# Optimization experiments

Hardware: AMD Instinct MI355X
Metric: run time of the kernel (lower is better)

The kernel has to match this reference:

```python
import jax, jax.numpy as jnp
import numpy as np

N_HEADS = 8
EMBED = 640
CROSS = 768
HEAD = EMBED // N_HEADS


def setup_inputs() -> dict:
    key = jax.random.key(0)
    ks = jax.random.split(key, 10)
    s_e = 1.0 / np.sqrt(EMBED)
    s_c = 1.0 / np.sqrt(CROSS)
    return {
        "x": jax.random.normal(ks[0], (8, 4096, EMBED), jnp.float32),
        "y": jax.random.normal(ks[1], (8, 77, CROSS), jnp.float32),
        "Wq": jax.random.uniform(ks[2], (EMBED, EMBED), jnp.float32, -s_e, s_e),
        "bq": jax.random.uniform(ks[3], (EMBED,), jnp.float32, -s_e, s_e),
        "Wk": jax.random.uniform(ks[4], (CROSS, EMBED), jnp.float32, -s_c, s_c),
        "bk": jax.random.uniform(ks[5], (EMBED,), jnp.float32, -s_c, s_c),
        "Wv": jax.random.uniform(ks[6], (CROSS, EMBED), jnp.float32, -s_c, s_c),
        "bv": jax.random.uniform(ks[7], (EMBED,), jnp.float32, -s_c, s_c),
        "Wo": jax.random.uniform(ks[8], (EMBED, EMBED), jnp.float32, -s_e, s_e),
        "bo": jax.random.uniform(ks[9], (EMBED,), jnp.float32, -s_e, s_e),
    }


def reference(x, y, Wq, bq, Wk, bk, Wv, bv, Wo, bo):
    B, T, C = x.shape
    S = y.shape[1]
    # projections; split heads: [B, H, T, D]
    q = (x @ Wq + bq).reshape(B, T, N_HEADS, HEAD).transpose(0, 2, 1, 3)
    k = (y @ Wk + bk).reshape(B, S, N_HEADS, HEAD).transpose(0, 2, 1, 3)
    v = (y @ Wv + bv).reshape(B, S, N_HEADS, HEAD).transpose(0, 2, 1, 3)
    scores = jnp.einsum("bhtd,bhsd->bhts", q, k) / jnp.sqrt(jnp.float32(HEAD))
    attn = jax.nn.softmax(scores, axis=-1)
    out = jnp.einsum("bhts,bhsd->bhtd", attn, v)
    out = out.transpose(0, 2, 1, 3).reshape(B, T, C)
    return out @ Wo + bo
```

## Files before the change

kernel.cpp:

```cpp
#include <hip/hip_runtime.h>
#include <hip/hip_bf16.h>
#include <hip/hip_fp16.h>

#define EMBED 640
#define CROSS 768
#define NH 8
#define HEAD 80
#define BATCH 8
#define SEQT 4096
#define SEQS 77
#define MROWS (BATCH * SEQT)

typedef _Float16 half8 __attribute__((ext_vector_type(8)));
typedef float floatx4 __attribute__((ext_vector_type(4)));

__device__ __forceinline__ void lds_load16(const void* g, void* l) {
    __builtin_amdgcn_global_load_lds(
        (const __attribute__((address_space(1))) void*)g,
        (__attribute__((address_space(3))) void*)l, 16, 0, 0);
}

__global__ __launch_bounds__(256) void cvt_f32_f16(
    const float* __restrict__ in, _Float16* __restrict__ out)
{
    size_t i = ((size_t)blockIdx.x * 256 + threadIdx.x) * 8;
    float4 a = *(const float4*)&in[i];
    float4 b = *(const float4*)&in[i + 4];
    half8 h;
    h[0] = (_Float16)a.x; h[1] = (_Float16)a.y;
    h[2] = (_Float16)a.z; h[3] = (_Float16)a.w;
    h[4] = (_Float16)b.x; h[5] = (_Float16)b.y;
    h[6] = (_Float16)b.z; h[7] = (_Float16)b.w;
    *(half8*)&out[i] = h;
}

__global__ __launch_bounds__(256) void cvt_y_f16(
    const float* __restrict__ y, _Float16* __restrict__ yh)
{
    size_t i = ((size_t)blockIdx.x * 256 + threadIdx.x) * 8;
    half8 h = {};
    if (i < (size_t)BATCH * SEQS * CROSS) {
        float4 a = *(const float4*)&y[i];
        float4 b = *(const float4*)&y[i + 4];
        h[0] = (_Float16)a.x; h[1] = (_Float16)a.y;
        h[2] = (_Float16)a.z; h[3] = (_Float16)a.w;
        h[4] = (_Float16)b.x; h[5] = (_Float16)b.y;
        h[6] = (_Float16)b.z; h[7] = (_Float16)b.w;
    }
    *(half8*)&yh[i] = h;
}

__global__ __launch_bounds__(256) void zero_f16(_Float16* __restrict__ p, size_t n8)
{
    size_t i = (size_t)blockIdx.x * 256 + threadIdx.x;
    if (i < n8) *(half8*)&p[i * 8] = (half8){};
}

__global__ __launch_bounds__(256) void transpose_cvt(
    const float* __restrict__ W, _Float16* __restrict__ Wt, int K, int N)
{
    __shared__ float t[32][33];
    const int k0 = blockIdx.y * 32, n0 = blockIdx.x * 32;
    for (int r = threadIdx.y; r < 32; r += 8)
        t[r][threadIdx.x] = W[(size_t)(k0 + r) * N + n0 + threadIdx.x];
    __syncthreads();
    for (int r = threadIdx.y; r < 32; r += 8)
        Wt[(size_t)(n0 + r) * K + k0 + threadIdx.x] = (_Float16)t[threadIdx.x][r];
}

template <bool HALF_OUT>
__global__ __launch_bounds__(256) void gemm_f16(
    const _Float16* __restrict__ A,
    const _Float16* __restrict__ Bt,
    const float* __restrict__ bias,
    void* __restrict__ Cout, int M, int N, int K, float scale)
{
    __shared__ _Float16 As[3][128 * 32];
    __shared__ _Float16 Bs[3][128 * 32];

    const int tid  = threadIdx.x;
    const int wave = tid >> 6;
    const int lane = tid & 63;
    const int quad = lane >> 4;
    const int l16  = lane & 15;

    const int l   = blockIdx.y * gridDim.x + blockIdx.x;
    const int inner = l >> 3;
    const int p   = (l & 7) + 8 * (inner / gridDim.x);
    const int nt  = inner % gridDim.x;
    const int m0 = p * 128, n0 = nt * 128;
    const int wm = (wave >> 1) * 64, wn = (wave & 1) * 64;

    const int row = tid >> 2;
    const int kch = ((tid & 3) ^ ((row >> 1) & 3)) * 8;
    const int cq  = (quad ^ ((l16 >> 1) & 3)) * 8;

    const _Float16* pa0 = &A [(size_t)(m0 + row)      * K + kch];
    const _Float16* pa1 = &A [(size_t)(m0 + 64 + row) * K + kch];
    const _Float16* pb0 = &Bt[(size_t)(n0 + row)      * K + kch];
    const _Float16* pb1 = &Bt[(size_t)(n0 + 64 + row) * K + kch];

    const int NT = K / 32;

    auto stage = [&](int t) {
        const int bf = t % 3;
        const int off = t * 32;
        lds_load16(pa0 + off, &As[bf][wave * 512]);
        lds_load16(pa1 + off, &As[bf][2048 + wave * 512]);
        lds_load16(pb0 + off, &Bs[bf][wave * 512]);
        lds_load16(pb1 + off, &Bs[bf][2048 + wave * 512]);
    };
    stage(0); stage(1); stage(2);

    floatx4 acc[4][4] = {};

    for (int t = 0; t < NT; ++t) {
        const int rem = NT - 1 - t;
        if (rem >= 2)      asm volatile("s_waitcnt vmcnt(8)" ::: "memory");
        else if (rem == 1) asm volatile("s_waitcnt vmcnt(4)" ::: "memory");
        else               asm volatile("s_waitcnt vmcnt(0)" ::: "memory");
        __builtin_amdgcn_s_barrier();

        const _Float16* as = As[t % 3];
        const _Float16* bs = Bs[t % 3];
        half8 a[4], b[4];
        #pragma unroll
        for (int i = 0; i < 4; ++i)
            a[i] = *(const half8*)&as[(wm + i * 16 + l16) * 32 + cq];
        #pragma unroll
        for (int j = 0; j < 4; ++j)
            b[j] = *(const half8*)&bs[(wn + j * 16 + l16) * 32 + cq];
        #pragma unroll
        for (int i = 0; i < 4; ++i)
            #pragma unroll
            for (int j = 0; j < 4; ++j)
                acc[i][j] = __builtin_amdgcn_mfma_f32_16x16x32_f16(
                    a[i], b[j], acc[i][j], 0, 0, 0);

        asm volatile("s_waitcnt lgkmcnt(0)" ::: "memory");
        __builtin_amdgcn_s_barrier();
        if (t + 3 < NT) stage(t + 3);
    }

    float bcol[4];
    #pragma unroll
    for (int j = 0; j < 4; ++j) bcol[j] = bias[n0 + wn + j * 16 + l16];
    #pragma unroll
    for (int i = 0; i < 4; ++i)
        #pragma unroll
        for (int r = 0; r < 4; ++r) {
            const int m = m0 + wm + i * 16 + quad * 4 + r;
            #pragma unroll
            for (int j = 0; j < 4; ++j) {
                float v = (acc[i][j][r] + bcol[j]) * scale;
                const size_t off = (size_t)m * N + n0 + wn + j * 16 + l16;
                if (HALF_OUT) ((_Float16*)Cout)[off] = (_Float16)v;
                else          ((float*)Cout)[off] = v;
            }
        }
}

__global__ __launch_bounds__(256) void kv_gemm(
    const _Float16* __restrict__ yh,
    const _Float16* __restrict__ Wkt, const _Float16* __restrict__ Wvt,
    const float* __restrict__ bk, const float* __restrict__ bv,
    _Float16* __restrict__ kh, _Float16* __restrict__ vth)
{
    __shared__ _Float16 As[64 * 32];
    __shared__ _Float16 Bs[64 * 32];

    const int tid = threadIdx.x;
    const int wave = tid >> 6, lane = tid & 63;
    const int quad = lane >> 4, l16 = lane & 15;
    const int m0 = blockIdx.y * 64, n0 = blockIdx.x * 64;
    const bool isV = blockIdx.z != 0;
    const _Float16* Bt = isV ? Wvt : Wkt;
    const float* bias  = isV ? bv : bk;

    const int row = tid >> 2;
    const int kch = (tid & 3) * 8;

    floatx4 acc[4] = {};

    for (int k0 = 0; k0 < CROSS; k0 += 32) {
        lds_load16(&yh[(size_t)(m0 + row) * CROSS + k0 + kch], &As[wave * 512]);
        lds_load16(&Bt[(size_t)(n0 + row) * CROSS + k0 + kch], &Bs[wave * 512]);
        __syncthreads();
        half8 b = *(const half8*)&Bs[(wave * 16 + l16) * 32 + quad * 8];
        #pragma unroll
        for (int i = 0; i < 4; ++i) {
            half8 a = *(const half8*)&As[(i * 16 + l16) * 32 + quad * 8];
            acc[i] = __builtin_amdgcn_mfma_f32_16x16x32_f16(a, b, acc[i], 0, 0, 0);
        }
        __syncthreads();
    }

    const int n = n0 + wave * 16 + l16;
    const int h = n / HEAD, d = n % HEAD;
    const float bb = bias[n];
    #pragma unroll
    for (int i = 0; i < 4; ++i)
        #pragma unroll
        for (int r = 0; r < 4; ++r) {
            const int m = m0 + i * 16 + quad * 4 + r;
            if (m >= BATCH * SEQS) continue;
            const int b_ = m / SEQS, s = m % SEQS;
            const int bh = b_ * NH + h;
            const float v = acc[i][r] + bb;
            if (isV) vth[(size_t)bh * (HEAD * 80) + d * 80 + s] = (_Float16)v;
            else     kh [(size_t)bh * (SEQS * HEAD) + s * HEAD + d] = (_Float16)v;
        }
}

__global__ __launch_bounds__(256, 4) void attn_mfma(
    const _Float16* __restrict__ qh,
    const _Float16* __restrict__ kh,
    const _Float16* __restrict__ vth,
    _Float16* __restrict__ oh)
{
    constexpr int LS = 88;
    __shared__ _Float16 lds[(80 + 80 + 64) * LS + 8];
    _Float16* Ks = lds;
    _Float16* Vt = lds + 80 * LS;
    _Float16* Ps = lds + 160 * LS;

    const int tid = threadIdx.x;
    const int wave = tid >> 6, lane = tid & 63;
    const int quad = lane >> 4, l16 = lane & 15;
    const int bh = blockIdx.y;
    const int b = bh >> 3, h = bh & 7;
    const size_t row0 = (size_t)b * SEQT + (size_t)blockIdx.x * 256;
    const half8 hz = {};

    const _Float16* qp = qh + (row0 + wave * 16 + l16) * EMBED + h * HEAD;

    half8 qa0 = *(const half8*)&qp[quad * 8];
    half8 qa1 = *(const half8*)&qp[32 + quad * 8];
    half8 qa2 = (quad < 2) ? *(const half8*)&qp[64 + quad * 8] : hz;

    for (int idx = tid; idx < 80 * 11; idx += 256) {
        const int s = idx / 11, c = idx % 11;
        half8 v = hz;
        if (s < SEQS && c < 10)
            v = *(const half8*)&kh[(size_t)bh * (SEQS * HEAD) + s * HEAD + c * 8];
        *(half8*)&Ks[s * LS + c * 8] = v;
    }
    for (int idx = tid; idx < 80 * 11; idx += 256) {
        const int d = idx / 11, c = idx % 11;
        half8 v = hz;
        if (c < 10)
            v = *(const half8*)&vth[(size_t)bh * (HEAD * 80) + d * 80 + c * 8];
        *(half8*)&Vt[d * LS + c * 8] = v;
    }
    __syncthreads();

    for (int t = 0; t < 4; ++t) {
        floatx4 accs[5] = {};
        #pragma unroll
        for (int st = 0; st < 5; ++st) {
            const _Float16* kr = &Ks[(st * 16 + l16) * LS];
            half8 b0 = *(const half8*)&kr[quad * 8];
            half8 b1 = *(const half8*)&kr[32 + quad * 8];
            half8 b2 = *(const half8*)&kr[64 + quad * 8];
            accs[st] = __builtin_amdgcn_mfma_f32_16x16x32_f16(qa0, b0, accs[st], 0, 0, 0);
            accs[st] = __builtin_amdgcn_mfma_f32_16x16x32_f16(qa1, b1, accs[st], 0, 0, 0);
            accs[st] = __builtin_amdgcn_mfma_f32_16x16x32_f16(qa2, b2, accs[st], 0, 0, 0);
        }
        if (l16 >= 13) {
            accs[4][0] = -1e30f; accs[4][1] = -1e30f;
            accs[4][2] = -1e30f; accs[4][3] = -1e30f;
        }

        float recip[4];
        #pragma unroll
        for (int r = 0; r < 4; ++r) {
            float m = accs[0][r];
            #pragma unroll
            for (int st = 1; st < 5; ++st) m = fmaxf(m, accs[st][r]);
            m = fmaxf(m, __shfl_xor(m, 1));
            m = fmaxf(m, __shfl_xor(m, 2));
            m = fmaxf(m, __shfl_xor(m, 4));
            m = fmaxf(m, __shfl_xor(m, 8));
            float l = 0.f;
            const int row = wave * 16 + quad * 4 + r;
            #pragma unroll
            for (int st = 0; st < 5; ++st) {
                float e = __expf(accs[st][r] - m);
                l += e;
                Ps[row * LS + st * 16 + l16] = (_Float16)e;
            }
            l += __shfl_xor(l, 1);
            l += __shfl_xor(l, 2);
            l += __shfl_xor(l, 4);
            l += __shfl_xor(l, 8);
            recip[r] = 1.0f / l;
        }
        __syncthreads();

        half8 qn0 = hz, qn1 = hz, qn2 = hz;
        if (t < 3) {
            const _Float16* qn = qp + (size_t)(t + 1) * 64 * EMBED;
            qn0 = *(const half8*)&qn[quad * 8];
            qn1 = *(const half8*)&qn[32 + quad * 8];
            if (quad < 2) qn2 = *(const half8*)&qn[64 + quad * 8];
        }

        const _Float16* pr = &Ps[(wave * 16 + l16) * LS];
        half8 pa0 = *(const half8*)&pr[quad * 8];
        half8 pa1 = *(const half8*)&pr[32 + quad * 8];
        half8 pa2 = (quad < 2) ? *(const half8*)&pr[64 + quad * 8] : hz;
        __syncthreads();

        floatx4 acco[5] = {};
        #pragma unroll
        for (int dt = 0; dt < 5; ++dt) {
            const _Float16* vr = &Vt[(dt * 16 + l16) * LS];
            half8 b0 = *(const half8*)&vr[quad * 8];
            half8 b1 = *(const half8*)&vr[32 + quad * 8];
            half8 b2 = *(const half8*)&vr[64 + quad * 8];
            acco[dt] = __builtin_amdgcn_mfma_f32_16x16x32_f16(pa0, b0, acco[dt], 0, 0, 0);
            acco[dt] = __builtin_amdgcn_mfma_f32_16x16x32_f16(pa1, b1, acco[dt], 0, 0, 0);
            acco[dt] = __builtin_amdgcn_mfma_f32_16x16x32_f16(pa2, b2, acco[dt], 0, 0, 0);
        }

        #pragma unroll
        for (int r = 0; r < 4; ++r) {
            const size_t grow = row0 + t * 64 + wave * 16 + quad * 4 + r;
            #pragma unroll
            for (int dt = 0; dt < 5; ++dt)
                oh[grow * EMBED + h * HEAD + dt * 16 + l16] =
                    (_Float16)(acco[dt][r] * recip[r]);
        }

        qa0 = qn0; qa1 = qn1; qa2 = qn2;
    }
}

extern "C" void kernel_launch(void* const* d_in, const int* in_sizes, int n_in,
                              void* d_out, int out_size, void* d_ws, size_t ws_size,
                              hipStream_t stream)
{
    const float* x  = (const float*)d_in[0];
    const float* y  = (const float*)d_in[1];
    const float* Wq = (const float*)d_in[2];
    const float* bq = (const float*)d_in[3];
    const float* Wk = (const float*)d_in[4];
    const float* bk = (const float*)d_in[5];
    const float* Wv = (const float*)d_in[6];
    const float* bv = (const float*)d_in[7];
    const float* Wo = (const float*)d_in[8];
    const float* bo = (const float*)d_in[9];
    float* out = (float*)d_out;

    const size_t ME = (size_t)MROWS * EMBED;
    _Float16* xh  = (_Float16*)d_ws;
    _Float16* qh  = xh + ME;
    _Float16* ah  = qh + ME;
    _Float16* kh  = ah + ME;
    _Float16* vth = kh  + (size_t)BATCH * NH * SEQS * HEAD;
    _Float16* wqt = vth + (size_t)BATCH * NH * HEAD * 80;
    _Float16* wot = wqt + (size_t)EMBED * EMBED;
    _Float16* yh  = wot + (size_t)EMBED * EMBED;
    _Float16* wkt = yh  + (size_t)640 * CROSS;
    _Float16* wvt = wkt + (size_t)EMBED * CROSS;

    cvt_f32_f16<<<dim3(ME / (256 * 8)), 256, 0, stream>>>(x, xh);
    transpose_cvt<<<dim3(EMBED / 32, EMBED / 32), dim3(32, 8), 0, stream>>>(Wq, wqt, EMBED, EMBED);
    transpose_cvt<<<dim3(EMBED / 32, EMBED / 32), dim3(32, 8), 0, stream>>>(Wo, wot, EMBED, EMBED);
    transpose_cvt<<<dim3(EMBED / 32, CROSS / 32), dim3(32, 8), 0, stream>>>(Wk, wkt, CROSS, EMBED);
    transpose_cvt<<<dim3(EMBED / 32, CROSS / 32), dim3(32, 8), 0, stream>>>(Wv, wvt, CROSS, EMBED);
    cvt_y_f16<<<dim3(640 * CROSS / (256 * 8)), 256, 0, stream>>>(y, yh);
    zero_f16<<<dim3(((size_t)BATCH * NH * HEAD * 80 / 8 + 255) / 256), 256, 0, stream>>>(
        vth, (size_t)BATCH * NH * HEAD * 80 / 8);

    gemm_f16<true><<<dim3(EMBED / 128, MROWS / 128), 256, 0, stream>>>(
        xh, wqt, bq, qh, MROWS, EMBED, EMBED, 0.11180339887498949f);
    kv_gemm<<<dim3(EMBED / 64, 640 / 64, 2), 256, 0, stream>>>(
        yh, wkt, wvt, bk, bv, kh, vth);
    attn_mfma<<<dim3(SEQT / 256, BATCH * NH), 256, 0, stream>>>(qh, kh, vth, ah);
    gemm_f16<false><<<dim3(EMBED / 128, MROWS / 128), 256, 0, stream>>>(
        ah, wot, bo, out, MROWS, EMBED, EMBED, 1.0f);
}
```

Baseline: 301.2 us.

## Fuse x conversion into Q GEMM, merge prep kernels, reschedule GEMM pipeline

The Q projection now reads fp32 x directly, converting to fp16 in registers before writing LDS. This removes the separate conversion pass and its fp16 round trip through global memory. The four weight transposes are merged into one launch, and the y conversion is merged with the V buffer zeroing, which cuts launch count. The output GEMM now issues its next stage right after the barrier with a two-ahead prefetch and drops the second barrier per k-step. The reuse of the third buffer in that GEMM, and the register-staged A loads in gemm_q, may create hazards or stalls.

```diff
diff --git a/kernel.cpp b/kernel.cpp
--- a/kernel.cpp
+++ b/kernel.cpp
@@ -20,47 +20,22 @@
         (__attribute__((address_space(3))) void*)l, 16, 0, 0);
 }
 
-__global__ __launch_bounds__(256) void cvt_f32_f16(
-    const float* __restrict__ in, _Float16* __restrict__ out)
-{
-    size_t i = ((size_t)blockIdx.x * 256 + threadIdx.x) * 8;
-    float4 a = *(const float4*)&in[i];
-    float4 b = *(const float4*)&in[i + 4];
-    half8 h;
-    h[0] = (_Float16)a.x; h[1] = (_Float16)a.y;
-    h[2] = (_Float16)a.z; h[3] = (_Float16)a.w;
-    h[4] = (_Float16)b.x; h[5] = (_Float16)b.y;
-    h[6] = (_Float16)b.z; h[7] = (_Float16)b.w;
-    *(half8*)&out[i] = h;
-}
-
-__global__ __launch_bounds__(256) void cvt_y_f16(
-    const float* __restrict__ y, _Float16* __restrict__ yh)
-{
-    size_t i = ((size_t)blockIdx.x * 256 + threadIdx.x) * 8;
-    half8 h = {};
-    if (i < (size_t)BATCH * SEQS * CROSS) {
-        float4 a = *(const float4*)&y[i];
-        float4 b = *(const float4*)&y[i + 4];
-        h[0] = (_Float16)a.x; h[1] = (_Float16)a.y;
-        h[2] = (_Float16)a.z; h[3] = (_Float16)a.w;
-        h[4] = (_Float16)b.x; h[5] = (_Float16)b.y;
-        h[6] = (_Float16)b.z; h[7] = (_Float16)b.w;
-    }
-    *(half8*)&yh[i] = h;
-}
-
-__global__ __launch_bounds__(256) void zero_f16(_Float16* __restrict__ p, size_t n8)
-{
-    size_t i = (size_t)blockIdx.x * 256 + threadIdx.x;
-    if (i < n8) *(half8*)&p[i * 8] = (half8){};
-}
-
-__global__ __launch_bounds__(256) void transpose_cvt(
-    const float* __restrict__ W, _Float16* __restrict__ Wt, int K, int N)
+__global__ __launch_bounds__(256) void transpose_all(
+    const float* __restrict__ Wq, const float* __restrict__ Wo,
+    const float* __restrict__ Wk, const float* __restrict__ Wv,
+    _Float16* __restrict__ wqt, _Float16* __restrict__ wot,
+    _Float16* __restrict__ wkt, _Float16* __restrict__ wvt)
 {
     __shared__ float t[32][33];
+    const int z = blockIdx.z;
+    const float* W;  _Float16* Wt;  int K;
+    if      (z == 0) { W = Wq; Wt = wqt; K = EMBED; }
+    else if (z == 1) { W = Wo; Wt = wot; K = EMBED; }
+    else if (z == 2) { W = Wk; Wt = wkt; K = CROSS; }
+    else             { W = Wv; Wt = wvt; K = CROSS; }
+    const int N = EMBED;
     const int k0 = blockIdx.y * 32, n0 = blockIdx.x * 32;
+    if (k0 >= K) return;
     for (int r = threadIdx.y; r < 32; r += 8)
         t[r][threadIdx.x] = W[(size_t)(k0 + r) * N + n0 + threadIdx.x];
     __syncthreads();
@@ -68,12 +43,34 @@
         Wt[(size_t)(n0 + r) * K + k0 + threadIdx.x] = (_Float16)t[threadIdx.x][r];
 }
 
-template <bool HALF_OUT>
+__global__ __launch_bounds__(256) void cvt_y_zero(
+    const float* __restrict__ y, _Float16* __restrict__ yh,
+    _Float16* __restrict__ vth)
+{
+    const size_t i = (size_t)blockIdx.x * 256 + threadIdx.x;
+    if (i < (size_t)640 * CROSS / 8) {
+        const size_t e = i * 8;
+        half8 h = {};
+        if (e < (size_t)BATCH * SEQS * CROSS) {
+            float4 a = *(const float4*)&y[e];
+            float4 b = *(const float4*)&y[e + 4];
+            h[0] = (_Float16)a.x; h[1] = (_Float16)a.y;
+            h[2] = (_Float16)a.z; h[3] = (_Float16)a.w;
+            h[4] = (_Float16)b.x; h[5] = (_Float16)b.y;
+            h[6] = (_Float16)b.z; h[7] = (_Float16)b.w;
+        }
+        *(half8*)&yh[e] = h;
+    } else {
+        const size_t j = (i - (size_t)640 * CROSS / 8) * 8;
+        *(half8*)&vth[j] = (half8){};
+    }
+}
+
 __global__ __launch_bounds__(256) void gemm_f16(
     const _Float16* __restrict__ A,
     const _Float16* __restrict__ Bt,
     const float* __restrict__ bias,
-    void* __restrict__ Cout, int M, int N, int K, float scale)
+    float* __restrict__ Cout, int M, int N, int K)
 {
     __shared__ _Float16 As[3][128 * 32];
     __shared__ _Float16 Bs[3][128 * 32];
@@ -110,16 +107,15 @@
         lds_load16(pb0 + off, &Bs[bf][wave * 512]);
         lds_load16(pb1 + off, &Bs[bf][2048 + wave * 512]);
     };
-    stage(0); stage(1); stage(2);
+    stage(0); stage(1);
 
     floatx4 acc[4][4] = {};
 
     for (int t = 0; t < NT; ++t) {
-        const int rem = NT - 1 - t;
-        if (rem >= 2)      asm volatile("s_waitcnt vmcnt(8)" ::: "memory");
-        else if (rem == 1) asm volatile("s_waitcnt vmcnt(4)" ::: "memory");
-        else               asm volatile("s_waitcnt vmcnt(0)" ::: "memory");
+        if (t < NT - 1) asm volatile("s_waitcnt vmcnt(4)" ::: "memory");
+        else            asm volatile("s_waitcnt vmcnt(0)" ::: "memory");
         __builtin_amdgcn_s_barrier();
+        if (t + 2 < NT) stage(t + 2);
 
         const _Float16* as = As[t % 3];
         const _Float16* bs = Bs[t % 3];
@@ -136,10 +132,6 @@
             for (int j = 0; j < 4; ++j)
                 acc[i][j] = __builtin_amdgcn_mfma_f32_16x16x32_f16(
                     a[i], b[j], acc[i][j], 0, 0, 0);
-
-        asm volatile("s_waitcnt lgkmcnt(0)" ::: "memory");
-        __builtin_amdgcn_s_barrier();
-        if (t + 3 < NT) stage(t + 3);
     }
 
     float bcol[4];
@@ -151,12 +143,125 @@
         for (int r = 0; r < 4; ++r) {
             const int m = m0 + wm + i * 16 + quad * 4 + r;
             #pragma unroll
-            for (int j = 0; j < 4; ++j) {
-                float v = (acc[i][j][r] + bcol[j]) * scale;
-                const size_t off = (size_t)m * N + n0 + wn + j * 16 + l16;
-                if (HALF_OUT) ((_Float16*)Cout)[off] = (_Float16)v;
-                else          ((float*)Cout)[off] = v;
-            }
+            for (int j = 0; j < 4; ++j)
+                Cout[(size_t)m * N + n0 + wn + j * 16 + l16] =
+                    acc[i][j][r] + bcol[j];
+        }
+}
+
+__global__ __launch_bounds__(256) void gemm_q(
+    const float* __restrict__ x,
+    const _Float16* __restrict__ Bt,
+    const float* __restrict__ bias,
+    _Float16* __restrict__ Cout)
+{
+    constexpr int K = EMBED, N = EMBED;
+    __shared__ _Float16 As[2][128 * 32];
+    __shared__ _Float16 Bs[2][128 * 32];
+
+    const int tid  = threadIdx.x;
+    const int wave = tid >> 6;
+    const int lane = tid & 63;
+    const int quad = lane >> 4;
+    const int l16  = lane & 15;
+
+    const int l   = blockIdx.y * gridDim.x + blockIdx.x;
+    const int inner = l >> 3;
+    const int p   = (l & 7) + 8 * (inner / gridDim.x);
+    const int nt  = inner % gridDim.x;
+    const int m0 = p * 128, n0 = nt * 128;
+    const int wm = (wave >> 1) * 64, wn = (wave & 1) * 64;
+
+    const int arow  = tid >> 1;
+    const int ahalf = tid & 1;
+    const int s_r   = (arow >> 1) & 3;
+    const int slot0 = ((ahalf * 2)     ^ s_r) * 8;
+    const int slot1 = ((ahalf * 2 + 1) ^ s_r) * 8;
+    const float* gx = &x[(size_t)(m0 + arow) * K + ahalf * 16];
+
+    const int brow = tid >> 2;
+    const int bkch = ((tid & 3) ^ ((brow >> 1) & 3)) * 8;
+    const _Float16* gb0 = &Bt[(size_t)(n0 + brow)      * K + bkch];
+    const _Float16* gb1 = &Bt[(size_t)(n0 + 64 + brow) * K + bkch];
+
+    const int cq = (quad ^ ((l16 >> 1) & 3)) * 8;
+
+    float4 f0, f1, f2, f3;
+    auto loadA = [&](int t) {
+        const float* gp = gx + t * 32;
+        f0 = *(const float4*)gp;       f1 = *(const float4*)(gp + 4);
+        f2 = *(const float4*)(gp + 8); f3 = *(const float4*)(gp + 12);
+    };
+    auto writeA = [&](int bf) {
+        half8 h0, h1;
+        h0[0] = (_Float16)f0.x; h0[1] = (_Float16)f0.y;
+        h0[2] = (_Float16)f0.z; h0[3] = (_Float16)f0.w;
+        h0[4] = (_Float16)f1.x; h0[5] = (_Float16)f1.y;
+        h0[6] = (_Float16)f1.z; h0[7] = (_Float16)f1.w;
+        h1[0] = (_Float16)f2.x; h1[1] = (_Float16)f2.y;
+        h1[2] = (_Float16)f2.z; h1[3] = (_Float16)f2.w;
+        h1[4] = (_Float16)f3.x; h1[5] = (_Float16)f3.y;
+        h1[6] = (_Float16)f3.z; h1[7] = (_Float16)f3.w;
+        *(half8*)&As[bf][arow * 32 + slot0] = h0;
+        *(half8*)&As[bf][arow * 32 + slot1] = h1;
+    };
+    auto loadB = [&](int t, int bf) {
+        lds_load16(gb0 + t * 32, &Bs[bf][wave * 512]);
+        lds_load16(gb1 + t * 32, &Bs[bf][2048 + wave * 512]);
+    };
+
+    constexpr int NT = K / 32;
+
+    loadB(0, 0); loadA(0);
+    asm volatile("s_waitcnt vmcnt(0)" ::: "memory");
+    writeA(0);
+    asm volatile("s_waitcnt lgkmcnt(0)" ::: "memory");
+    __builtin_amdgcn_s_barrier();
+
+    floatx4 acc[4][4] = {};
+    int cur = 0;
+
+    for (int t = 0; t < NT; ++t) {
+        if (t + 1 < NT) { loadB(t + 1, cur ^ 1); loadA(t + 1); }
+
+        const _Float16* as = As[cur];
+        const _Float16* bs = Bs[cur];
+        half8 a[4], b[4];
+        #pragma unroll
+        for (int i = 0; i < 4; ++i)
+            a[i] = *(const half8*)&as[(wm + i * 16 + l16) * 32 + cq];
+        #pragma unroll
+        for (int j = 0; j < 4; ++j)
+            b[j] = *(const half8*)&bs[(wn + j * 16 + l16) * 32 + cq];
+        #pragma unroll
+        for (int i = 0; i < 4; ++i)
+            #pragma unroll
+            for (int j = 0; j < 4; ++j)
+                acc[i][j] = __builtin_amdgcn_mfma_f32_16x16x32_f16(
+                    a[i], b[j], acc[i][j], 0, 0, 0);
+
+        if (t + 1 < NT) {
+            asm volatile("s_waitcnt vmcnt(0)" ::: "memory");
+            writeA(cur ^ 1);
+            asm volatile("s_waitcnt lgkmcnt(0)" ::: "memory");
+        }
+        __builtin_amdgcn_s_barrier();
+        cur ^= 1;
+    }
+
+    const float scale = 0.11180339887498949f;
+    float bcol[4];
+    #pragma unroll
+    for (int j = 0; j < 4; ++j) bcol[j] = bias[n0 + wn + j * 16 + l16];
+    #pragma unroll
+    for (int i = 0; i < 4; ++i)
+        #pragma unroll
+        for (int r = 0; r < 4; ++r) {
+            const int m = m0 + wm + i * 16 + quad * 4 + r;
+            #pragma unroll
+            for (int j = 0; j < 4; ++j)
+                Cout[(size_t)m * N + n0 + wn + j * 16 + l16] =
+                    (_Float16)((acc[i][j][r] + bcol[j]) * scale);
         }
 }
 
@@ -353,8 +458,7 @@
     float* out = (float*)d_out;
 
     const size_t ME = (size_t)MROWS * EMBED;
-    _Float16* xh  = (_Float16*)d_ws;
-    _Float16* qh  = xh + ME;
+    _Float16* qh  = (_Float16*)d_ws;
     _Float16* ah  = qh + ME;
     _Float16* kh  = ah + ME;
     _Float16* vth = kh  + (size_t)BATCH * NH * SEQS * HEAD;
@@ -364,20 +468,14 @@
     _Float16* wkt = yh  + (size_t)640 * CROSS;
     _Float16* wvt = wkt + (size_t)EMBED * CROSS;
 
-    cvt_f32_f16<<<dim3(ME / (256 * 8)), 256, 0, stream>>>(x, xh);
-    transpose_cvt<<<dim3(EMBED / 32, EMBED / 32), dim3(32, 8), 0, stream>>>(Wq, wqt, EMBED, EMBED);
-    transpose_cvt<<<dim3(EMBED / 32, EMBED / 32), dim3(32, 8), 0, stream>>>(Wo, wot, EMBED, EMBED);
-    transpose_cvt<<<dim3(EMBED / 32, CROSS / 32), dim3(32, 8), 0, stream>>>(Wk, wkt, CROSS, EMBED);
-    transpose_cvt<<<dim3(EMBED / 32, CROSS / 32), dim3(32, 8), 0, stream>>>(Wv, wvt, CROSS, EMBED);
-    cvt_y_f16<<<dim3(640 * CROSS / (256 * 8)), 256, 0, stream>>>(y, yh);
-    zero_f16<<<dim3(((size_t)BATCH * NH * HEAD * 80 / 8 + 255) / 256), 256, 0, stream>>>(
-        vth, (size_t)BATCH * NH * HEAD * 80 / 8);
-
-    gemm_f16<true><<<dim3(EMBED / 128, MROWS / 128), 256, 0, stream>>>(
-        xh, wqt, bq, qh, MROWS, EMBED, EMBED, 0.11180339887498949f);
+    transpose_all<<<dim3(EMBED / 32, CROSS / 32, 4), dim3(32, 8), 0, stream>>>(
+        Wq, Wo, Wk, Wv, wqt, wot, wkt, wvt);
+    cvt_y_zero<<<dim3(440), 256, 0, stream>>>(y, yh, vth);
+
+    gemm_q<<<dim3(EMBED / 128, MROWS / 128), 256, 0, stream>>>(x, wqt, bq, qh);
     kv_gemm<<<dim3(EMBED / 64, 640 / 64, 2), 256, 0, stream>>>(
         yh, wkt, wvt, bk, bv, kh, vth);
     attn_mfma<<<dim3(SEQT / 256, BATCH * NH), 256, 0, stream>>>(qh, kh, vth, ah);
-    gemm_f16<false><<<dim3(EMBED / 128, MROWS / 128), 256, 0, stream>>>(
-        ah, wot, bo, out, MROWS, EMBED, EMBED, 1.0f);
-}
+    gemm_f16<<<dim3(EMBED / 128, MROWS / 128), 256, 0, stream>>>(
+        ah, wot, bo, out, MROWS, EMBED, EMBED);
+}
```

Measured after the change: 313.0 us. 1.04x slower.
